# Kernel optimization log

Hardware: AMD Instinct MI355X
Metric: run time of the kernel (lower is better)

## Reference

```python
import jax, jax.numpy as jnp
from jax import lax
import numpy as np

NUM_KIND = 4
V, H, B = 34, 32, 4096   # raw vertical (2 rows dropped), horizontal, batch
KS = 33                  # odd-rounded max(V-2, H)
NUM_DEPTH = 4
N_SQ = 100


def _conv(x, w):
    # x: (N,1,h,w), w: (1,1,KS,KS); torch Conv2d == cross-correlation == lax default
    return lax.conv_general_dilated(x, w, (1, 1), 'SAME',
                                    dimension_numbers=('NCHW', 'OIHW', 'NCHW'))


def _conv_k(x, w):
    # x: (K,B,1,h,w) -> conv each map with the shared 1-channel kernel
    k, b, c, h, wd = x.shape
    return _conv(x.reshape(k * b, c, h, wd), w).reshape(k, b, c, h, wd)


def setup_inputs() -> dict:
    key = jax.random.key(0)
    ks = jax.random.split(key, 8)
    std = 0.3
    return {
        'dots':    jax.random.randint(ks[0], (V, H, B), 0, NUM_KIND + 1, dtype=jnp.int32),
        'w_each':  jax.random.normal(ks[1], (1, 1, KS, KS), jnp.float32) * std,
        'w_not':   jax.random.normal(ks[2], (1, 1, KS, KS), jnp.float32) * std,
        'w_not2':  jax.random.normal(ks[3], (1, 1, KS, KS), jnp.float32) * std,
        'w_empty': jax.random.normal(ks[4], (1, 1, KS, KS), jnp.float32) * std,
        'W1':      jax.random.normal(ks[5], (N_SQ, (V - 2) * H), jnp.float32) * std,
        'W2':      jax.random.normal(ks[6], (N_SQ, N_SQ), jnp.float32) * std,
        'W3':      jax.random.normal(ks[7], (1, N_SQ), jnp.float32) * std,
    }


def reference(dots, w_each, w_not, w_not2, w_empty, W1, W2, W3):
    # drop last 2 vertical rows, layout (V-2,H,B) -> (B,1,V-2,H)
    board = dots[:-2].astype(jnp.float32).transpose(2, 0, 1)[:, None]  # (B,1,h,w)

    empty = (board == 0).astype(jnp.float32)
    E = _conv(empty, w_empty)                                           # (B,1,h,w)

    kinds = jnp.arange(1, NUM_KIND + 1, dtype=board.dtype).reshape(NUM_KIND, 1, 1, 1, 1)
    each = (board[None] == kinds).astype(jnp.float32)                   # (K,B,1,h,w)
    notm = ((each + empty[None]) == 0).astype(jnp.float32)              # (K,B,1,h,w)

    # first pass: per-color value, masked to that color's cells
    notm_conv = _conv_k(notm, w_not)      # note: the torch code LOGS the convolved not-mask
    v = _conv_k(each, w_each) + E[None] - notm_conv
    L = each * v                          # each_color_value_log (masked)
    s = jax.nn.sigmoid(L.sum(axis=0))     # all_color_value_2nd, (B,1,h,w)

    # iterative diffusion; torch mutates the log in-place each depth:
    # L <- mask * (L + E + conv2nd(notm_conv * before)); before is detached
    for _ in range(NUM_DEPTH):
        before = lax.stop_gradient(s)
        C = _conv_k(notm_conv * before[None], w_not2)
        L = each * (L + E[None] + C)
        s = jax.nn.sigmoid(L.sum(axis=0))

    feat = s.reshape(s.shape[0], -1)      # (B, (V-2)*H)
    x = jax.nn.leaky_relu(feat @ W1.T, 0.2)
    x = jax.nn.leaky_relu(x @ W2.T, 0.2)
    return x @ W3.T                        # (B,1)
```

## Files before the change

### kernel.cpp

```cpp
#include <hip/hip_runtime.h>
#include <cstdint>
#include <cstddef>


typedef _Float16 f16;
typedef __attribute__((ext_vector_type(8))) _Float16 f16x8;
typedef __attribute__((ext_vector_type(4))) float f32x4;

#define NB   4096
#define PIX  1024
#define MR   (NB * 4)

__device__ __forceinline__ void gld_lds16(const void* g, void* l) {
    __builtin_amdgcn_global_load_lds(
        (const __attribute__((address_space(1))) void*)g,
        (__attribute__((address_space(3))) void*)l, 16, 0, 0);
}

__global__ void build_mats(const float* __restrict__ we, const float* __restrict__ wn,
                           const float* __restrict__ wn2, const float* __restrict__ wem,
                           f16* __restrict__ Me, f16* __restrict__ Mn,
                           f16* __restrict__ Mn2, f16* __restrict__ Mem) {
    int idx = blockIdx.x * 256 + threadIdx.x;
    int o = idx >> 10, in = idx & 1023;
    int i = o >> 5, j = o & 31, a = in >> 5, b = in & 31;
    int u = a - i + 16, v = b - j + 16;
    bool ok = (u >= 0) && (u < 33) && (v >= 0) && (v < 33);
    int w = u * 33 + v;
    float ve = 0.f, vn = 0.f, vn2 = 0.f, vem = 0.f;
    if (ok) { ve = we[w]; vn = wn[w]; vn2 = wn2[w]; vem = wem[w]; }
    Me[idx]  = (f16)ve;
    Mn[idx]  = (f16)vn;
    Mn2[idx] = (f16)vn2;
    Mem[idx] = (f16)vem;
}

__global__ void build_w1(const float* __restrict__ W1, f16* __restrict__ W1b) {
    int idx = blockIdx.x * 256 + threadIdx.x;
    int j = idx >> 10, i = idx & 1023;
    W1b[idx] = (f16)(j < 100 ? W1[j * 1024 + i] : 0.f);
}

__global__ void build_board(const int* __restrict__ dots, unsigned char* __restrict__ board) {
    __shared__ unsigned char tile[64][68];
    int t = threadIdx.x;
    int bp = blockIdx.x & 15, bn = blockIdx.x >> 4;
    int p0 = bp * 64, n0 = bn * 64;
    int ln = t & 63, lp = t >> 6;
#pragma unroll
    for (int j = 0; j < 16; j++) {
        int p = lp * 16 + j;
        tile[p][ln] = (unsigned char)dots[(size_t)(p0 + p) * 4096 + n0 + ln];
    }
    __syncthreads();
#pragma unroll
    for (int j = 0; j < 16; j++) {
        int n = lp * 16 + j;
        board[(size_t)(n0 + n) * 1024 + p0 + ln] = tile[ln][n];
    }
}

__global__ void mk_sa(const f16* __restrict__ S1sel, const f16* __restrict__ En,
                      const f16* __restrict__ NC,
                      const unsigned char* __restrict__ board,
                      f16* __restrict__ Lsel, f16* __restrict__ Sa) {
    int idx = blockIdx.x * 256 + threadIdx.x;
    int n = idx >> 10, o = idx & 1023;
    int c = board[idx];
    float L = 0.f;
    if (c > 0) {
        float ncsel = (float)NC[(size_t)(4 * n + c - 1) * 1024 + o];
        L = (float)S1sel[idx] + (float)En[idx] - ncsel;
    }
    Lsel[idx] = (f16)L;
    Sa[idx] = (f16)(1.f / (1.f + __expf(-L)));
}

template <int MODE, int ASRC>
__device__ __forceinline__ void run_gemm(
    int bjob, int ypx, int nx, char* smem,
    const f16* __restrict__ X, const f16* __restrict__ B,
    const unsigned char* __restrict__ board,
    f16* __restrict__ outB, int ldo, float* __restrict__ outF) {
    char* smB = smem;
    char* smA = smem + 16384;

    const int tid = threadIdx.x;
    const int wv = tid >> 6, ln = tid & 63;
    const int wm = wv >> 1, wn_ = wv & 1;
    const int lr = ln & 15, lq = ln >> 4;

    int xcd = bjob & 7, slot = bjob >> 3;
    int bx = slot % nx;
    int by = xcd * ypx + slot / nx;
    const int rtile = by * 128, otile = bx * 128;
    const int img0 = (ASRC == 4) ? rtile : (rtile >> 2);

    const f32x4 fz = {0.f, 0.f, 0.f, 0.f};
    f32x4 acc[4][4];
#pragma unroll
    for (int i = 0; i < 4; i++)
#pragma unroll
        for (int j = 0; j < 4; j++) acc[i][j] = fz;

    for (int kb = 0; kb < 1024; kb += 64) {
#pragma unroll
        for (int t = 0; t < 4; t++) {
            int c = (wv * 4 + t) * 64 + ln;
            int row = c >> 3, gcol = (c & 7) ^ (row & 7);
            gld_lds16(B + (size_t)(otile + row) * 1024 + kb + gcol * 8, smB + c * 16);
        }
        if (ASRC == 0) {
#pragma unroll
            for (int t = 0; t < 4; t++) {
                int c = (wv * 4 + t) * 64 + ln;
                int row = c >> 3, gcol = (c & 7) ^ (row & 7);
                gld_lds16(X + (size_t)(rtile + row) * 1024 + kb + gcol * 8, smA + c * 16);
            }
        } else if (ASRC == 4) {
#pragma unroll
            for (int t = 0; t < 2; t++) {
                int c = t * 256 + wv * 64 + ln;
                int row = c >> 2, g = (c & 3) ^ (row & 3);
                gld_lds16(board + (size_t)(img0 + row) * 1024 + kb + g * 16, smA + c * 16);
            }
        } else {
            if (wv < 2) {
                int c = wv * 64 + ln;
                int row = c >> 2, g = (c & 3) ^ (row & 3);
                gld_lds16(board + (size_t)(img0 + row) * 1024 + kb + g * 16, smA + c * 16);
            }
        }
        __syncthreads();

#pragma unroll
        for (int kk = 0; kk < 2; kk++) {
            const int oct = kk * 4 + lq;
            f16x8 af[4], bfr[4];
#pragma unroll
            for (int i = 0; i < 4; i++) {
                int rrow = wm * 64 + i * 16 + lr;
                if (ASRC == 0) {
                    af[i] = *(const f16x8*)(smA + rrow * 128 + (oct ^ (rrow & 7)) * 16);
                } else {
                    int m = (ASRC == 4) ? rrow : (rrow >> 2);
                    int k1 = (rrow & 3) + 1;
                    uint64_t bb = *(const uint64_t*)(smA + m * 64 +
                                    ((oct >> 1) ^ (m & 3)) * 16 + (oct & 1) * 8);
                    f16x8 v;
#pragma unroll
                    for (int jj = 0; jj < 8; jj++) {
                        int bj = (int)((bb >> (8 * jj)) & 0xff);
                        bool on = (ASRC == 2) ? (bj == k1)
                                : (ASRC == 3) ? (bj != 0 && bj != k1)
                                              : (bj == 0);
                        v[jj] = on ? (f16)1.f : (f16)0.f;
                    }
                    af[i] = v;
                }
            }
#pragma unroll
            for (int j = 0; j < 4; j++) {
                int brow = wn_ * 64 + j * 16 + lr;
                bfr[j] = *(const f16x8*)(smB + brow * 128 + (oct ^ (brow & 7)) * 16);
            }
#pragma unroll
            for (int i = 0; i < 4; i++)
#pragma unroll
                for (int j = 0; j < 4; j++)
                    acc[i][j] = __builtin_amdgcn_mfma_f32_16x16x32_f16(
                        af[i], bfr[j], acc[i][j], 0, 0, 0);
        }
        __syncthreads();
    }

#pragma unroll
    for (int i = 0; i < 4; i++) {
        int rbase = rtile + wm * 64 + i * 16 + lq * 4;
#pragma unroll
        for (int j = 0; j < 4; j++) {
            int o = otile + wn_ * 64 + j * 16 + lr;
            f32x4 a = acc[i][j];
            if (MODE == 0) {
#pragma unroll
                for (int v = 0; v < 4; v++)
                    outB[(size_t)(rbase + v) * ldo + o] = (f16)a[v];
            } else if (MODE == 5) {
#pragma unroll
                for (int v = 0; v < 4; v++) {
                    float x = a[v];
                    outF[(size_t)(rbase + v) * ldo + o] = x > 0.f ? x : 0.2f * x;
                }
            } else {
                int n = rbase >> 2;
                size_t no = (size_t)n * PIX + o;
                int c = board[no];
                float asel = (c == 1) ? a[0] : (c == 2) ? a[1] : (c == 3) ? a[2] : a[3];
                outB[no] = (f16)asel;
            }
        }
    }
}

__global__ void __launch_bounds__(256, 4) gemm_fa(
    const f16* __restrict__ Me, const f16* __restrict__ Mn,
    const f16* __restrict__ Mem, const unsigned char* __restrict__ board,
    f16* __restrict__ S1sel, f16* __restrict__ NC, f16* __restrict__ En) {
    __shared__ __attribute__((aligned(16))) char smem[24576];
    int bi = blockIdx.x;
    if (bi < 1024) {
        run_gemm<1, 2>(bi, 16, 8, smem, nullptr, Me, board, S1sel, 0, nullptr);
    } else if (bi < 2048) {
        run_gemm<0, 3>(bi - 1024, 16, 8, smem, nullptr, Mn, board, NC, PIX, nullptr);
    } else {
        run_gemm<0, 4>(bi - 2048, 4, 8, smem, nullptr, Mem, board, En, PIX, nullptr);
    }
}

template <int MODE>
__global__ void __launch_bounds__(256, 2) gemm_depth(
    const f16* __restrict__ Mn2, const unsigned char* __restrict__ board,
    const f16* __restrict__ NCs, const f16* __restrict__ Sin,
    const f16* __restrict__ En, f16* __restrict__ Lsel,
    f16* __restrict__ outB) {
    __shared__ __attribute__((aligned(16))) char smem[32768];
    char* smB = smem;
    char* smA = smem + 16384;

    const int tid = threadIdx.x;
    const int wv = tid >> 6, ln = tid & 63;
    const int wm = wv >> 1, wn_ = wv & 1;
    const int lr = ln & 15, lq = ln >> 4;

    int bi = blockIdx.x;
    int xcd = bi & 7, slot = bi >> 3;
    int bx = slot & 7;
    int by = xcd * 16 + (slot >> 3);
    const int rtile = by * 128, otile = bx * 128;

    const f16* ncp[4];
    const f16* sp[4];
#pragma unroll
    for (int t = 0; t < 4; t++) {
        int c = (wv * 4 + t) * 64 + ln;
        int row = c >> 3, gcol = (c & 7) ^ (row & 7);
        int gr = rtile + row;
        ncp[t] = NCs + (size_t)gr * 1024 + gcol * 8;
        sp[t]  = Sin + (size_t)(gr >> 2) * 1024 + gcol * 8;
    }

    const f32x4 fz = {0.f, 0.f, 0.f, 0.f};
    f32x4 acc[4][4];
#pragma unroll
    for (int i = 0; i < 4; i++)
#pragma unroll
        for (int j = 0; j < 4; j++) acc[i][j] = fz;

    f16x8 pNC[4], pS[4];
#pragma unroll
    for (int t = 0; t < 4; t++) {
        pNC[t] = *(const f16x8*)(ncp[t]);
        pS[t]  = *(const f16x8*)(sp[t]);
    }

    for (int kb = 0; kb < 1024; kb += 64) {
#pragma unroll
        for (int t = 0; t < 4; t++) {
            int c = (wv * 4 + t) * 64 + ln;
            *(f16x8*)(smA + c * 16) = pNC[t] * pS[t];
        }
#pragma unroll
        for (int t = 0; t < 4; t++) {
            int c = (wv * 4 + t) * 64 + ln;
            int row = c >> 3, gcol = (c & 7) ^ (row & 7);
            gld_lds16(Mn2 + (size_t)(otile + row) * 1024 + kb + gcol * 8, smB + c * 16);
        }
        __syncthreads();

        if (kb + 64 < 1024) {
#pragma unroll
            for (int t = 0; t < 4; t++) {
                pNC[t] = *(const f16x8*)(ncp[t] + kb + 64);
                pS[t]  = *(const f16x8*)(sp[t] + kb + 64);
            }
        }

#pragma unroll
        for (int kk = 0; kk < 2; kk++) {
            const int oct = kk * 4 + lq;
            f16x8 af[4], bfr[4];
#pragma unroll
            for (int i = 0; i < 4; i++) {
                int rrow = wm * 64 + i * 16 + lr;
                af[i] = *(const f16x8*)(smA + rrow * 128 + (oct ^ (rrow & 7)) * 16);
            }
#pragma unroll
            for (int j = 0; j < 4; j++) {
                int brow = wn_ * 64 + j * 16 + lr;
                bfr[j] = *(const f16x8*)(smB + brow * 128 + (oct ^ (brow & 7)) * 16);
            }
#pragma unroll
            for (int i = 0; i < 4; i++)
#pragma unroll
                for (int j = 0; j < 4; j++)
                    acc[i][j] = __builtin_amdgcn_mfma_f32_16x16x32_f16(
                        af[i], bfr[j], acc[i][j], 0, 0, 0);
        }
        __syncthreads();
    }

#pragma unroll
    for (int i = 0; i < 4; i++) {
        int rbase = rtile + wm * 64 + i * 16 + lq * 4;
#pragma unroll
        for (int j = 0; j < 4; j++) {
            int o = otile + wn_ * 64 + j * 16 + lr;
            f32x4 a = acc[i][j];
            int n = rbase >> 2;
            size_t no = (size_t)n * PIX + o;
            int c = board[no];
            float asel = (c == 1) ? a[0] : (c == 2) ? a[1] : (c == 3) ? a[2] : a[3];
            float E = (float)En[no];
            float Lnew = (c > 0) ? ((float)Lsel[no] + E + asel) : 0.f;
            float s = 1.f / (1.f + __expf(-Lnew));
            if (MODE != 4) Lsel[no] = (f16)Lnew;
            outB[no] = (f16)s;
        }
    }
}

__global__ void __launch_bounds__(256, 4) gemm_mlp(
    const f16* __restrict__ feat, const f16* __restrict__ W1b,
    float* __restrict__ X1) {
    __shared__ __attribute__((aligned(16))) char smem[32768];
    run_gemm<5, 0>(blockIdx.x, 4, 1, smem, feat, W1b, nullptr, nullptr, 128, X1);
}

__global__ void __launch_bounds__(256) mlp23(const float* __restrict__ X1,
                                             const float* __restrict__ W2,
                                             const float* __restrict__ W3,
                                             float* __restrict__ out) {
    __shared__ float sW2[10000];
    __shared__ float sW3[100];
    __shared__ float red[256];
    int t = threadIdx.x;
    for (int idx = t; idx < 10000; idx += 256) sW2[idx] = W2[idx];
    if (t < 100) sW3[t] = W3[t];
    __syncthreads();
    int nb = t >> 2, q = t & 3;
    int n = blockIdx.x * 64 + nb;
    const float* x1 = X1 + (size_t)n * 128;
    float xr[100];
#pragma unroll
    for (int i = 0; i < 100; i++) xr[i] = x1[i];
    float partial = 0.f;
    for (int jj = 0; jj < 25; jj++) {
        int j = q + jj * 4;
        const float* w2r = sW2 + j * 100;
        float acc2 = 0.f;
#pragma unroll
        for (int i = 0; i < 100; i++) acc2 += w2r[i] * xr[i];
        partial += sW3[j] * (acc2 > 0.f ? acc2 : 0.2f * acc2);
    }
    red[t] = partial;
    __syncthreads();
    if (q == 0) out[n] = red[t] + red[t + 1] + red[t + 2] + red[t + 3];
}

extern "C" void kernel_launch(void* const* d_in, const int* in_sizes, int n_in,
                              void* d_out, int out_size, void* d_ws, size_t ws_size,
                              hipStream_t stream) {
    (void)in_sizes; (void)n_in; (void)out_size; (void)ws_size;
    const int*   dots   = (const int*)d_in[0];
    const float* w_each = (const float*)d_in[1];
    const float* w_not  = (const float*)d_in[2];
    const float* w_not2 = (const float*)d_in[3];
    const float* w_emp  = (const float*)d_in[4];
    const float* W1 = (const float*)d_in[5];
    const float* W2 = (const float*)d_in[6];
    const float* W3 = (const float*)d_in[7];
    float* out = (float*)d_out;

    char* ws = (char*)d_ws;
    size_t off = 0;
    auto alloc = [&](size_t bytes) -> char* {
        char* p = ws + off;
        off += (bytes + 255) & ~(size_t)255;
        return p;
    };
    f16* Me    = (f16*)alloc((size_t)PIX * PIX * 2);
    f16* Mn    = (f16*)alloc((size_t)PIX * PIX * 2);
    f16* Mn2   = (f16*)alloc((size_t)PIX * PIX * 2);
    f16* Mem   = (f16*)alloc((size_t)PIX * PIX * 2);
    f16* W1b   = (f16*)alloc((size_t)128 * PIX * 2);
    unsigned char* board = (unsigned char*)alloc((size_t)NB * PIX);
    f16* NC    = (f16*)alloc((size_t)MR * PIX * 2);
    f16* En    = (f16*)alloc((size_t)NB * PIX * 2);
    f16* S1sel = (f16*)alloc((size_t)NB * PIX * 2);
    f16* Sa    = (f16*)alloc((size_t)NB * PIX * 2);
    f16* Sb    = (f16*)alloc((size_t)NB * PIX * 2);
    f16* feat  = (f16*)alloc((size_t)NB * PIX * 2);
    f16* Lsel  = (f16*)alloc((size_t)NB * PIX * 2);
    float* X1  = (float*)alloc((size_t)NB * 128 * 4);

    build_board<<<1024, 256, 0, stream>>>(dots, board);
    build_mats<<<4096, 256, 0, stream>>>(w_each, w_not, w_not2, w_emp,
                                         Me, Mn, Mn2, Mem);
    build_w1<<<512, 256, 0, stream>>>(W1, W1b);

    dim3 blk(256);
    gemm_fa<<<2304, blk, 0, stream>>>(Me, Mn, Mem, board, S1sel, NC, En);
    mk_sa<<<16384, blk, 0, stream>>>(S1sel, En, NC, board, Lsel, Sa);
    gemm_depth<3><<<1024, blk, 0, stream>>>(Mn2, board, NC, Sa, En, Lsel, Sb);
    gemm_depth<3><<<1024, blk, 0, stream>>>(Mn2, board, NC, Sb, En, Lsel, Sa);
    gemm_depth<3><<<1024, blk, 0, stream>>>(Mn2, board, NC, Sa, En, Lsel, Sb);
    gemm_depth<4><<<1024, blk, 0, stream>>>(Mn2, board, NC, Sb, En, Lsel, feat);
    gemm_mlp<<<32, blk, 0, stream>>>(feat, W1b, X1);
    mlp23<<<64, blk, 0, stream>>>(X1, W2, W3, out);
}
```

Before: 452.4 us.

## Precompute NC*s products in epilogue and stream A operand via direct LDS loads

The A operand of the depth GEMMs (not-conv times previous sigmoid) is now formed in the previous kernel's epilogue and written as a full (4B x 1024) fp16 matrix. The GEMM main loop then loads it straight into LDS with global_load_lds instead of doing register loads, a multiply and an LDS store. The log-state Lsel is also switched to fp32, for better accuracy. The cost is extra global writes of the 4x-sized product matrix and extra NC reads in each epilogue, with less ALU and register pressure in the main loop.

```diff
diff --git a/kernel.cpp b/kernel.cpp
--- a/kernel.cpp
+++ b/kernel.cpp
@@ -63,17 +63,23 @@
 __global__ void mk_sa(const f16* __restrict__ S1sel, const f16* __restrict__ En,
                       const f16* __restrict__ NC,
                       const unsigned char* __restrict__ board,
-                      f16* __restrict__ Lsel, f16* __restrict__ Sa) {
+                      float* __restrict__ Lsel, f16* __restrict__ P1) {
     int idx = blockIdx.x * 256 + threadIdx.x;
     int n = idx >> 10, o = idx & 1023;
     int c = board[idx];
+    size_t r0 = (size_t)(4 * n) * PIX + o;
+    f16 nc0 = NC[r0], nc1 = NC[r0 + PIX], nc2 = NC[r0 + 2 * PIX], nc3 = NC[r0 + 3 * PIX];
     float L = 0.f;
     if (c > 0) {
-        float ncsel = (float)NC[(size_t)(4 * n + c - 1) * 1024 + o];
+        float ncsel = (float)((c == 1) ? nc0 : (c == 2) ? nc1 : (c == 3) ? nc2 : nc3);
         L = (float)S1sel[idx] + (float)En[idx] - ncsel;
     }
-    Lsel[idx] = (f16)L;
-    Sa[idx] = (f16)(1.f / (1.f + __expf(-L)));
+    Lsel[idx] = L;
+    f16 s = (f16)(1.f / (1.f + __expf(-L)));
+    P1[r0]           = nc0 * s;
+    P1[r0 + PIX]     = nc1 * s;
+    P1[r0 + 2 * PIX] = nc2 * s;
+    P1[r0 + 3 * PIX] = nc3 * s;
 }
 
 template <int MODE, int ASRC>
@@ -219,10 +225,10 @@
 
 template <int MODE>
 __global__ void __launch_bounds__(256, 2) gemm_depth(
-    const f16* __restrict__ Mn2, const unsigned char* __restrict__ board,
-    const f16* __restrict__ NCs, const f16* __restrict__ Sin,
-    const f16* __restrict__ En, f16* __restrict__ Lsel,
-    f16* __restrict__ outB) {
+    const f16* __restrict__ Pin, const f16* __restrict__ Mn2,
+    const unsigned char* __restrict__ board, const f16* __restrict__ NC,
+    const f16* __restrict__ En, float* __restrict__ Lsel,
+    f16* __restrict__ Pout, f16* __restrict__ feat) {
     __shared__ __attribute__((aligned(16))) char smem[32768];
     char* smB = smem;
     char* smA = smem + 16384;
@@ -238,17 +244,6 @@
     int by = xcd * 16 + (slot >> 3);
     const int rtile = by * 128, otile = bx * 128;
 
-    const f16* ncp[4];
-    const f16* sp[4];
-#pragma unroll
-    for (int t = 0; t < 4; t++) {
-        int c = (wv * 4 + t) * 64 + ln;
-        int row = c >> 3, gcol = (c & 7) ^ (row & 7);
-        int gr = rtile + row;
-        ncp[t] = NCs + (size_t)gr * 1024 + gcol * 8;
-        sp[t]  = Sin + (size_t)(gr >> 2) * 1024 + gcol * 8;
-    }
-
     const f32x4 fz = {0.f, 0.f, 0.f, 0.f};
     f32x4 acc[4][4];
 #pragma unroll
@@ -256,34 +251,15 @@
 #pragma unroll
         for (int j = 0; j < 4; j++) acc[i][j] = fz;
 
-    f16x8 pNC[4], pS[4];
-#pragma unroll
-    for (int t = 0; t < 4; t++) {
-        pNC[t] = *(const f16x8*)(ncp[t]);
-        pS[t]  = *(const f16x8*)(sp[t]);
-    }
-
     for (int kb = 0; kb < 1024; kb += 64) {
-#pragma unroll
-        for (int t = 0; t < 4; t++) {
-            int c = (wv * 4 + t) * 64 + ln;
-            *(f16x8*)(smA + c * 16) = pNC[t] * pS[t];
-        }
 #pragma unroll
         for (int t = 0; t < 4; t++) {
             int c = (wv * 4 + t) * 64 + ln;
             int row = c >> 3, gcol = (c & 7) ^ (row & 7);
             gld_lds16(Mn2 + (size_t)(otile + row) * 1024 + kb + gcol * 8, smB + c * 16);
+            gld_lds16(Pin + (size_t)(rtile + row) * 1024 + kb + gcol * 8, smA + c * 16);
         }
         __syncthreads();
-
-        if (kb + 64 < 1024) {
-#pragma unroll
-            for (int t = 0; t < 4; t++) {
-                pNC[t] = *(const f16x8*)(ncp[t] + kb + 64);
-                pS[t]  = *(const f16x8*)(sp[t] + kb + 64);
-            }
-        }
 
 #pragma unroll
         for (int kk = 0; kk < 2; kk++) {
@@ -321,10 +297,19 @@
             int c = board[no];
             float asel = (c == 1) ? a[0] : (c == 2) ? a[1] : (c == 3) ? a[2] : a[3];
             float E = (float)En[no];
-            float Lnew = (c > 0) ? ((float)Lsel[no] + E + asel) : 0.f;
+            float Lnew = (c > 0) ? (Lsel[no] + E + asel) : 0.f;
             float s = 1.f / (1.f + __expf(-Lnew));
-            if (MODE != 4) Lsel[no] = (f16)Lnew;
-            outB[no] = (f16)s;
+            if (MODE == 4) {
+                feat[no] = (f16)s;
+            } else {
+                Lsel[no] = Lnew;
+                f16 sh = (f16)s;
+                size_t r0 = (size_t)rbase * PIX + o;
+                Pout[r0]           = NC[r0] * sh;
+                Pout[r0 + PIX]     = NC[r0 + PIX] * sh;
+                Pout[r0 + 2 * PIX] = NC[r0 + 2 * PIX] * sh;
+                Pout[r0 + 3 * PIX] = NC[r0 + 3 * PIX] * sh;
+            }
         }
     }
 }
@@ -397,10 +382,10 @@
     f16* NC    = (f16*)alloc((size_t)MR * PIX * 2);
     f16* En    = (f16*)alloc((size_t)NB * PIX * 2);
     f16* S1sel = (f16*)alloc((size_t)NB * PIX * 2);
-    f16* Sa    = (f16*)alloc((size_t)NB * PIX * 2);
-    f16* Sb    = (f16*)alloc((size_t)NB * PIX * 2);
+    f16* Pa    = (f16*)alloc((size_t)MR * PIX * 2);
+    f16* Pb    = (f16*)alloc((size_t)MR * PIX * 2);
     f16* feat  = (f16*)alloc((size_t)NB * PIX * 2);
-    f16* Lsel  = (f16*)alloc((size_t)NB * PIX * 2);
+    float* Lsel= (float*)alloc((size_t)NB * PIX * 4);
     float* X1  = (float*)alloc((size_t)NB * 128 * 4);
 
     build_board<<<1024, 256, 0, stream>>>(dots, board);
@@ -410,11 +395,11 @@
 
     dim3 blk(256);
     gemm_fa<<<2304, blk, 0, stream>>>(Me, Mn, Mem, board, S1sel, NC, En);
-    mk_sa<<<16384, blk, 0, stream>>>(S1sel, En, NC, board, Lsel, Sa);
-    gemm_depth<3><<<1024, blk, 0, stream>>>(Mn2, board, NC, Sa, En, Lsel, Sb);
-    gemm_depth<3><<<1024, blk, 0, stream>>>(Mn2, board, NC, Sb, En, Lsel, Sa);
-    gemm_depth<3><<<1024, blk, 0, stream>>>(Mn2, board, NC, Sa, En, Lsel, Sb);
-    gemm_depth<4><<<1024, blk, 0, stream>>>(Mn2, board, NC, Sb, En, Lsel, feat);
+    mk_sa<<<16384, blk, 0, stream>>>(S1sel, En, NC, board, Lsel, Pa);
+    gemm_depth<3><<<1024, blk, 0, stream>>>(Pa, Mn2, board, NC, En, Lsel, Pb, nullptr);
+    gemm_depth<3><<<1024, blk, 0, stream>>>(Pb, Mn2, board, NC, En, Lsel, Pa, nullptr);
+    gemm_depth<3><<<1024, blk, 0, stream>>>(Pa, Mn2, board, NC, En, Lsel, Pb, nullptr);
+    gemm_depth<4><<<1024, blk, 0, stream>>>(Pb, Mn2, board, NC, En, Lsel, nullptr, feat);
     gemm_mlp<<<32, blk, 0, stream>>>(feat, W1b, X1);
     mlp23<<<64, blk, 0, stream>>>(X1, W2, W3, out);
 }
```

New measurement: 417.9 us. -7.6%, faster.
